# Kernel tuning notes

Measured on AMD Instinct MI355X. Metric: run time of the kernel, lower is better.

Reference implementation:

```python
import jax, jax.numpy as jnp
import numpy as np

N_NODES = 50000
N_EDGES = 1600000
D = 128
N_GRAPHS = 64


def gcn_conv(x, row, col, deg_inv_sqrt, W, b):
    # GCNConv: out_i = sum_{j->i} norm_ij * (x_j @ W) + norm_ii * (x_i @ W) + b
    # with self-loops folded in and norm_ij = d_i^{-1/2} d_j^{-1/2}
    h = x @ W  # [N, H]
    norm = deg_inv_sqrt[row] * deg_inv_sqrt[col]  # [E]
    msg = h[row] * norm[:, None]  # gather over source nodes
    agg = jax.ops.segment_sum(msg, col, num_segments=N_NODES)
    agg = agg + h * (deg_inv_sqrt * deg_inv_sqrt)[:, None]  # self-loop term
    return agg + b


def setup_inputs() -> dict:
    key = jax.random.key(0)
    ks = jax.random.split(key, 12)
    x = jax.random.normal(ks[0], (N_NODES, D), dtype=jnp.float32)
    edge_index = jax.random.randint(ks[1], (2, N_EDGES), 0, N_NODES, dtype=jnp.int32)
    batch = jnp.sort(jax.random.randint(ks[2], (N_NODES,), 0, N_GRAPHS, dtype=jnp.int32))
    s = 1.0 / np.sqrt(D)
    W1 = jax.random.uniform(ks[3], (D, D), jnp.float32, -s, s)
    b1 = jax.random.uniform(ks[4], (D,), jnp.float32, -s, s)
    W2 = jax.random.uniform(ks[5], (D, D), jnp.float32, -s, s)
    b2 = jax.random.uniform(ks[6], (D,), jnp.float32, -s, s)
    W3 = jax.random.uniform(ks[7], (D, D), jnp.float32, -s, s)
    b3 = jax.random.uniform(ks[8], (D,), jnp.float32, -s, s)
    Wf = jax.random.uniform(ks[9], (D, 1), jnp.float32, -s, s)
    bf = jax.random.uniform(ks[10], (1,), jnp.float32, -s, s)
    return {"x": x, "edge_index": edge_index, "batch": batch,
            "W1": W1, "b1": b1, "W2": W2, "b2": b2, "W3": W3, "b3": b3,
            "Wf": Wf, "bf": bf}


def reference(x, edge_index, batch, W1, b1, W2, b2, W3, b3, Wf, bf):
    row, col = edge_index[0], edge_index[1]  # source -> target
    ones = jnp.ones((N_EDGES,), dtype=jnp.float32)
    deg = jax.ops.segment_sum(ones, col, num_segments=N_NODES) + 1.0  # +1 self-loop
    deg_inv_sqrt = jax.lax.rsqrt(deg)

    h = x
    for W, b in ((W1, b1), (W2, b2), (W3, b3)):
        h = gcn_conv(h, row, col, deg_inv_sqrt, W, b)
        h = jax.nn.relu(h)  # dropout is identity in eval mode (p=0)

    # global mean pool over graphs
    sums = jax.ops.segment_sum(h, batch, num_segments=N_GRAPHS)
    counts = jax.ops.segment_sum(jnp.ones((N_NODES,), jnp.float32), batch, num_segments=N_GRAPHS)
    pooled = sums / jnp.maximum(counts, 1.0)[:, None]  # [G, D]

    out = pooled @ Wf + bf  # [G, 1]
    return jax.nn.sigmoid(out)
```

## Files before the change

kernel.cpp:

```cpp
#include <hip/hip_runtime.h>
#include <hip/hip_fp16.h>
#include <math.h>

#define N_NODES 50000
#define N_EDGES 1600000
#define DIM     128
#define N_GRAPHS 64

typedef unsigned int uint32;
typedef __attribute__((ext_vector_type(8))) short bf16x8;
typedef __attribute__((ext_vector_type(4))) float f32x4;

static __device__ __forceinline__ ushort f2b(float f) {
    uint32 u = __float_as_uint(f);
    uint32 r = (u + 0x7fffu + ((u >> 16) & 1u)) >> 16;
    return (ushort)r;
}
static __device__ __forceinline__ float b2f(ushort h) {
    return __uint_as_float(((uint32)h) << 16);
}
static __device__ __forceinline__ unsigned char f2e5(float f) {
    ushort hb = __half_as_ushort(__float2half(f));
    return (unsigned char)(((uint32)hb + 0x7fu + ((hb >> 8) & 1u)) >> 8);
}
union h2u_t { uint32 u; __half2 h; };
static __device__ __forceinline__ __half2 u2h2(uint32 u) { h2u_t t; t.u = u; return t.h; }
static __device__ __forceinline__ uint32 h2u(__half2 h)  { h2u_t t; t.h = h; return t.u; }
static __device__ __forceinline__ __half2 dec01(uint32 v) {
    return u2h2(__builtin_amdgcn_perm(v, 0u, 0x05000400u));
}
static __device__ __forceinline__ __half2 dec23(uint32 v) {
    return u2h2(__builtin_amdgcn_perm(v, 0u, 0x07000600u));
}
static __device__ __forceinline__ int permf(int p) { return ((p & 7) << 4) + (p >> 3); }

#define NBUK 196
#define CAP  16384
#define PB1  512
#define CHUNK1 (N_EDGES / PB1)

__global__ __launch_bounds__(256) void prep_k(const float* __restrict__ W1,
                                              const float* __restrict__ W2,
                                              const float* __restrict__ W3,
                                              ushort* __restrict__ wt,
                                              int* __restrict__ gfill,
                                              float* __restrict__ pooled) {
    int blk = blockIdx.x;
    if (blk < 192) {
        int w = blk >> 6;
        const float* W = (w == 0) ? W1 : (w == 1) ? W2 : W3;
        ushort* o = wt + w * (DIM * DIM);
        int t = (blk & 63) * 256 + threadIdx.x;
        int n = t >> 7, kp = t & 127;
        int f = (w == 0) ? kp : permf(kp);
        o[n * 128 + kp] = f2b(W[f * 128 + n]);
    } else if (blk == 192) {
        int t = threadIdx.x;
        if (t < NBUK) gfill[t] = t * CAP;
    } else {
        int t = (blk - 193) * 256 + threadIdx.x;
        if (t < N_GRAPHS * DIM + N_GRAPHS) pooled[t] = 0.f;
    }
}

__global__ __launch_bounds__(256) void bin_k(const int* __restrict__ col,
                                             const int* __restrict__ row,
                                             int* __restrict__ gfill,
                                             uint32* __restrict__ packed) {
    __shared__ int hist[NBUK];
    __shared__ int cur[NBUK];
    int tid = threadIdx.x;
    for (int t = tid; t < NBUK; t += 256) hist[t] = 0;
    __syncthreads();
    int start = blockIdx.x * CHUNK1, end = start + CHUNK1;
    for (int e = start + tid; e < end; e += 256)
        atomicAdd(&hist[col[e] >> 8], 1);
    __syncthreads();
    for (int t = tid; t < NBUK; t += 256) {
        int h = hist[t];
        cur[t] = h ? atomicAdd(&gfill[t], h) : 0;
    }
    __syncthreads();
    for (int e = start + tid; e < end; e += 256) {
        int c = col[e];
        int r = row[e];
        int pos = atomicAdd(&cur[c >> 8], 1);
        packed[pos] = ((uint32)(c & 255) << 16) | (uint32)r;
    }
}

__global__ __launch_bounds__(256) void bucket_k(const uint32* __restrict__ packed,
                                                const int* __restrict__ gfill,
                                                int* __restrict__ cnt,
                                                int* __restrict__ offs,
                                                float* __restrict__ dis,
                                                ushort* __restrict__ csr) {
    __shared__ int bsm[256];
    __shared__ int hist[256];
    __shared__ int sm[256];
    __shared__ int lo[256];
    __shared__ int rank[256];
    int b = blockIdx.x, tid = threadIdx.x;

    int bsz = (tid < NBUK) ? (gfill[tid] - tid * CAP) : 0;
    bsm[tid] = bsz;
    __syncthreads();
    for (int off = 1; off < 256; off <<= 1) {
        int u = 0;
        if (tid >= off) u = bsm[tid - off];
        __syncthreads();
        if (tid >= off) bsm[tid] += u;
        __syncthreads();
    }
    int size = gfill[b] - b * CAP;
    int gb = bsm[b] - size;

    const uint32* pk = packed + (size_t)b * CAP;
    hist[tid] = 0; rank[tid] = 0;
    __syncthreads();
    for (int e = tid; e < size; e += 256) atomicAdd(&hist[pk[e] >> 16], 1);
    __syncthreads();
    int h = hist[tid];
    sm[tid] = h;
    __syncthreads();
    for (int off = 1; off < 256; off <<= 1) {
        int u = 0;
        if (tid >= off) u = sm[tid - off];
        __syncthreads();
        if (tid >= off) sm[tid] += u;
        __syncthreads();
    }
    lo[tid] = sm[tid] - h;
    int node = (b << 8) + tid;
    if (node < N_NODES) {
        cnt[node]  = h;
        offs[node] = gb + lo[tid];
        dis[node]  = rsqrtf((float)h + 1.0f);
    }
    __syncthreads();
    for (int e = tid; e < size; e += 256) {
        uint32 p = pk[e];
        int cl = p >> 16;
        int r = atomicAdd(&rank[cl], 1);
        csr[gb + lo[cl] + r] = (ushort)(p & 0xffffu);
    }
}

__global__ __launch_bounds__(256) void conv_k(const float* __restrict__ x, ushort* __restrict__ xb) {
    int i = blockIdx.x * blockDim.x + threadIdx.x;
    const int n4 = N_NODES * DIM / 4;
    if (i >= n4) return;
    float4 v = ((const float4*)x)[i];
    ushort4 o;
    o.x = f2b(v.x); o.y = f2b(v.y); o.z = f2b(v.z); o.w = f2b(v.w);
    ((ushort4*)xb)[i] = o;
}

__global__ __launch_bounds__(256) void gemm_mfma_k(const ushort* __restrict__ xb,
                                                   const ushort* __restrict__ wt,
                                                   const float* __restrict__ dis,
                                                   unsigned char* __restrict__ gb) {
    int wid  = threadIdx.x >> 6;
    int lane = threadIdx.x & 63;
    int r0 = blockIdx.x * 128 + wid * 32;
    int m  = lane & 15;
    int kg = lane >> 4;

    int arow0 = r0 + m;
    int arow1 = r0 + 16 + m;
    if (arow0 >= N_NODES) arow0 = N_NODES - 1;
    if (arow1 >= N_NODES) arow1 = N_NODES - 1;
    const ushort* abase0 = xb + (size_t)arow0 * DIM + kg * 8;
    const ushort* abase1 = xb + (size_t)arow1 * DIM + kg * 8;
    const ushort* wbase  = wt + (size_t)m * DIM + kg * 8;

    f32x4 acc[2][8];
    #pragma unroll
    for (int hh = 0; hh < 2; ++hh)
        #pragma unroll
        for (int nt = 0; nt < 8; ++nt) acc[hh][nt] = (f32x4){0.f, 0.f, 0.f, 0.f};

    #pragma unroll
    for (int kb = 0; kb < 4; ++kb) {
        bf16x8 a0 = *(const bf16x8*)(abase0 + kb * 32);
        bf16x8 a1 = *(const bf16x8*)(abase1 + kb * 32);
        #pragma unroll
        for (int nt = 0; nt < 8; ++nt) {
            bf16x8 b = *(const bf16x8*)(wbase + (size_t)nt * 16 * DIM + kb * 32);
            acc[0][nt] = __builtin_amdgcn_mfma_f32_16x16x32_bf16(a0, b, acc[0][nt], 0, 0, 0);
            acc[1][nt] = __builtin_amdgcn_mfma_f32_16x16x32_bf16(a1, b, acc[1][nt], 0, 0, 0);
        }
    }

    #pragma unroll
    for (int hh = 0; hh < 2; ++hh) {
        int orow0 = r0 + hh * 16 + kg * 4;
        #pragma unroll
        for (int i = 0; i < 4; ++i) {
            int rr = orow0 + i;
            if (rr >= N_NODES) continue;
            float dsc = dis[rr];
            uint32 u0 = (uint32)f2e5(acc[hh][0][i] * dsc)
                      | ((uint32)f2e5(acc[hh][1][i] * dsc) << 8)
                      | ((uint32)f2e5(acc[hh][2][i] * dsc) << 16)
                      | ((uint32)f2e5(acc[hh][3][i] * dsc) << 24);
            uint32 u1 = (uint32)f2e5(acc[hh][4][i] * dsc)
                      | ((uint32)f2e5(acc[hh][5][i] * dsc) << 8)
                      | ((uint32)f2e5(acc[hh][6][i] * dsc) << 16)
                      | ((uint32)f2e5(acc[hh][7][i] * dsc) << 24);
            uint2 u = make_uint2(u0, u1);
            *(uint2*)(gb + (size_t)rr * DIM + m * 8) = u;
        }
    }
}

__global__ __launch_bounds__(256) void agg_k(const unsigned char* __restrict__ gb,
                                             const float* __restrict__ dis,
                                             const ushort* __restrict__ csr,
                                             const int* __restrict__ offs,
                                             const int* __restrict__ cnt,
                                             const float* __restrict__ bias,
                                             ushort* __restrict__ outb) {
    int lane = threadIdx.x & 63;
    int node = blockIdx.x * 4 + (threadIdx.x >> 6);
    if (node >= N_NODES) return;
    int hi = lane >> 5;
    uint32 c4 = (uint32)(lane & 31) << 2;
    const unsigned char* gq = gb + c4;

    uint32 sv = *(const uint32*)(gq + ((uint32)node << 7));
    if (hi) sv = 0;
    __half2 a0 = dec01(sv), b0 = dec23(sv);
    __half2 a1 = u2h2(0),   b1 = u2h2(0);

    int base = offs[node];
    int c = cnt[node];
    for (int s0 = 0; s0 < c; s0 += 64) {
        int rem = c - s0;
        int m = rem < 64 ? rem : 64;
        int idx = 0;
        if (lane < m) idx = csr[base + s0 + lane];
        int t = 0;
        for (; t + 16 <= m; t += 16) {
            uint32 v[8];
            #pragma unroll
            for (int p = 0; p < 8; ++p) {
                int j0 = __shfl(idx, t + 2 * p, 64);
                int j1 = __shfl(idx, t + 2 * p + 1, 64);
                int jr = hi ? j1 : j0;
                v[p] = *(const uint32*)(gq + ((uint32)jr << 7));
            }
            #pragma unroll
            for (int p = 0; p < 8; ++p) {
                if (p & 1) { a1 = __hadd2(a1, dec01(v[p])); b1 = __hadd2(b1, dec23(v[p])); }
                else       { a0 = __hadd2(a0, dec01(v[p])); b0 = __hadd2(b0, dec23(v[p])); }
            }
        }
        for (; t + 2 <= m; t += 2) {
            int j0 = __shfl(idx, t, 64);
            int j1 = __shfl(idx, t + 1, 64);
            int jr = hi ? j1 : j0;
            uint32 v = *(const uint32*)(gq + ((uint32)jr << 7));
            a0 = __hadd2(a0, dec01(v)); b0 = __hadd2(b0, dec23(v));
        }
        if (t < m) {
            int j = __shfl(idx, t, 64);
            uint32 v = *(const uint32*)(gq + ((uint32)j << 7));
            if (hi) v = 0;
            a0 = __hadd2(a0, dec01(v)); b0 = __hadd2(b0, dec23(v));
        }
    }

    __half2 accA = __hadd2(a0, a1);
    __half2 accB = __hadd2(b0, b1);
    accA = __hadd2(accA, u2h2((uint32)__shfl_xor((int)h2u(accA), 32, 64)));
    accB = __hadd2(accB, u2h2((uint32)__shfl_xor((int)h2u(accB), 32, 64)));

    if (hi == 0) {
        float f0 = __low2float(accA), f1 = __high2float(accA);
        float f2 = __low2float(accB), f3 = __high2float(accB);
        float d = dis[node];
        float bv0 = bias[permf(c4 + 0)];
        float bv1 = bias[permf(c4 + 1)];
        float bv2 = bias[permf(c4 + 2)];
        float bv3 = bias[permf(c4 + 3)];
        ushort4 o;
        o.x = f2b(fmaxf(fmaf(f0, d, bv0), 0.f));
        o.y = f2b(fmaxf(fmaf(f1, d, bv1), 0.f));
        o.z = f2b(fmaxf(fmaf(f2, d, bv2), 0.f));
        o.w = f2b(fmaxf(fmaf(f3, d, bv3), 0.f));
        *(ushort4*)(outb + ((size_t)node << 7) + c4) = o;
    }
}

#define POOL_BLOCKS 1024
__global__ __launch_bounds__(128) void pool_k(const ushort* __restrict__ hb,
                                              const int* __restrict__ batch,
                                              float* __restrict__ pooled,
                                              float* __restrict__ counts) {
    const int chunk = (N_NODES + POOL_BLOCKS - 1) / POOL_BLOCKS;
    int tid = threadIdx.x;
    int start = blockIdx.x * chunk;
    int end = start + chunk; if (end > N_NODES) end = N_NODES;
    if (start >= end) return;

    float acc = 0.f;
    int cur = batch[start];
    int cl = 0;
    for (int n = start; n < end; ++n) {
        int b = batch[n];
        if (b != cur) {
            atomicAdd(&pooled[cur * DIM + tid], acc);
            if (tid == 0) atomicAdd(&counts[cur], (float)cl);
            acc = 0.f; cl = 0; cur = b;
        }
        acc += b2f(hb[((size_t)n << 7) + tid]);
        ++cl;
    }
    atomicAdd(&pooled[cur * DIM + tid], acc);
    if (tid == 0) atomicAdd(&counts[cur], (float)cl);
}

__global__ void final_k(const float* __restrict__ pooled, const float* __restrict__ counts,
                        const float* __restrict__ Wf, const float* __restrict__ bf,
                        float* __restrict__ out) {
    __shared__ float sred[2];
    int gidx = blockIdx.x;
    int tid = threadIdx.x;
    float c = fmaxf(counts[gidx], 1.0f);
    float v = pooled[gidx * DIM + tid] / c * Wf[permf(tid)];
    for (int off = 32; off > 0; off >>= 1) v += __shfl_down(v, off, 64);
    if ((tid & 63) == 0) sred[tid >> 6] = v;
    __syncthreads();
    if (tid == 0) {
        float t = sred[0] + sred[1] + bf[0];
        out[gidx] = 1.0f / (1.0f + expf(-t));
    }
}

extern "C" void kernel_launch(void* const* d_in, const int* in_sizes, int n_in,
                              void* d_out, int out_size, void* d_ws, size_t ws_size,
                              hipStream_t stream) {
    const float* x     = (const float*)d_in[0];
    const int*   ei    = (const int*)d_in[1];
    const int*   batch = (const int*)d_in[2];
    const float* W1 = (const float*)d_in[3];  const float* b1 = (const float*)d_in[4];
    const float* W2 = (const float*)d_in[5];  const float* b2 = (const float*)d_in[6];
    const float* W3 = (const float*)d_in[7];  const float* b3 = (const float*)d_in[8];
    const float* Wf = (const float*)d_in[9];  const float* bf = (const float*)d_in[10];
    const int* rowp = ei;
    const int* colp = ei + N_EDGES;

    char* ws = (char*)d_ws;
    size_t o = 0;
    auto alloc = [&](size_t bytes) -> void* {
        void* p = ws + o;
        o += (bytes + 255) & ~(size_t)255;
        return p;
    };
    int*    cnt    = (int*)   alloc((size_t)N_NODES * 4);
    int*    offs   = (int*)   alloc((size_t)N_NODES * 4);
    int*    gfill  = (int*)   alloc(256 * 4);
    float*  dis    = (float*) alloc((size_t)N_NODES * 4);
    ushort* csr    = (ushort*)alloc((size_t)N_EDGES * 2);
    uint32* packed = (uint32*)alloc((size_t)NBUK * CAP * 4);
    float*  pooled = (float*) alloc((size_t)(N_GRAPHS * DIM + N_GRAPHS) * 4);
    ushort* wt     = (ushort*)alloc((size_t)3 * DIM * DIM * 2);
    unsigned char* bufA = (unsigned char*)alloc((size_t)N_NODES * DIM);
    ushort* bufB   = (ushort*)alloc((size_t)N_NODES * DIM * 2);
    float*  counts = pooled + N_GRAPHS * DIM;

    prep_k<<<226, 256, 0, stream>>>(W1, W2, W3, wt, gfill, pooled);
    bin_k<<<PB1, 256, 0, stream>>>(colp, rowp, gfill, packed);
    bucket_k<<<NBUK, 256, 0, stream>>>(packed, gfill, cnt, offs, dis, csr);

    conv_k<<<(N_NODES * DIM / 4 + 255) / 256, 256, 0, stream>>>(x, bufB);

    const int GB = (N_NODES + 127) / 128;

    gemm_mfma_k<<<GB, 256, 0, stream>>>(bufB, wt, dis, bufA);
    agg_k<<<(N_NODES + 3) / 4, 256, 0, stream>>>(bufA, dis, csr, offs, cnt, b1, bufB);
    gemm_mfma_k<<<GB, 256, 0, stream>>>(bufB, wt + DIM * DIM, dis, bufA);
    agg_k<<<(N_NODES + 3) / 4, 256, 0, stream>>>(bufA, dis, csr, offs, cnt, b2, bufB);
    gemm_mfma_k<<<GB, 256, 0, stream>>>(bufB, wt + 2 * DIM * DIM, dis, bufA);
    agg_k<<<(N_NODES + 3) / 4, 256, 0, stream>>>(bufA, dis, csr, offs, cnt, b3, bufB);

    pool_k<<<POOL_BLOCKS, 128, 0, stream>>>(bufB, batch, pooled, counts);
    final_k<<<N_GRAPHS, 128, 0, stream>>>(pooled, counts, Wf, bf, (float*)d_out);
}
```

Measured before the change: 239.5 us.

## Fuse x conversion into prep, cache edges in LDS, pack fp8 via cvt_pkrtz

Moves the fp32-to-bf16 conversion of x into the prep kernel, removing one kernel launch. bin_k now stages each block's col/row pairs in shared memory so the edge arrays are read from global memory once instead of twice. The GEMM epilogue replaces per-element fp16-to-e5 rounding with a packed cvt_pkrtz conversion plus byte permutes, cutting ALU work in the epilogue. The packed conversion rounds toward zero to fp16 before the e5m2 rounding step, which may slightly change numerics versus round-to-nearest.

```diff
diff --git a/kernel.cpp b/kernel.cpp
--- a/kernel.cpp
+++ b/kernel.cpp
@@ -22,6 +22,12 @@
 static __device__ __forceinline__ unsigned char f2e5(float f) {
     ushort hb = __half_as_ushort(__float2half(f));
     return (unsigned char)(((uint32)hb + 0x7fu + ((hb >> 8) & 1u)) >> 8);
+}
+static __device__ __forceinline__ uint32 pk2(float a, float b) {
+    auto h = __builtin_amdgcn_cvt_pkrtz(a, b);
+    uint32 u;
+    __builtin_memcpy(&u, &h, 4);
+    return u + 0x007F007Fu + ((u >> 8) & 0x00010001u);
 }
 union h2u_t { uint32 u; __half2 h; };
 static __device__ __forceinline__ __half2 u2h2(uint32 u) { h2u_t t; t.u = u; return t.h; }
@@ -39,53 +45,69 @@
 #define PB1  512
 #define CHUNK1 (N_EDGES / PB1)
 
-__global__ __launch_bounds__(256) void prep_k(const float* __restrict__ W1,
+#define PREP_CONV 6250
+__global__ __launch_bounds__(256) void prep_k(const float* __restrict__ x,
+                                              ushort* __restrict__ xb,
+                                              const float* __restrict__ W1,
                                               const float* __restrict__ W2,
                                               const float* __restrict__ W3,
                                               ushort* __restrict__ wt,
                                               int* __restrict__ gfill,
                                               float* __restrict__ pooled) {
     int blk = blockIdx.x;
-    if (blk < 192) {
-        int w = blk >> 6;
+    if (blk < PREP_CONV) {
+        int i = blk * 256 + threadIdx.x;
+        float4 v = ((const float4*)x)[i];
+        ushort4 o;
+        o.x = f2b(v.x); o.y = f2b(v.y); o.z = f2b(v.z); o.w = f2b(v.w);
+        ((ushort4*)xb)[i] = o;
+    } else if (blk < PREP_CONV + 192) {
+        int b2 = blk - PREP_CONV;
+        int w = b2 >> 6;
         const float* W = (w == 0) ? W1 : (w == 1) ? W2 : W3;
         ushort* o = wt + w * (DIM * DIM);
-        int t = (blk & 63) * 256 + threadIdx.x;
+        int t = (b2 & 63) * 256 + threadIdx.x;
         int n = t >> 7, kp = t & 127;
         int f = (w == 0) ? kp : permf(kp);
         o[n * 128 + kp] = f2b(W[f * 128 + n]);
-    } else if (blk == 192) {
+    } else if (blk == PREP_CONV + 192) {
         int t = threadIdx.x;
         if (t < NBUK) gfill[t] = t * CAP;
     } else {
-        int t = (blk - 193) * 256 + threadIdx.x;
+        int t = (blk - (PREP_CONV + 193)) * 256 + threadIdx.x;
         if (t < N_GRAPHS * DIM + N_GRAPHS) pooled[t] = 0.f;
     }
 }
+#define PREP_BLOCKS (PREP_CONV + 193 + 33)
 
 __global__ __launch_bounds__(256) void bin_k(const int* __restrict__ col,
                                              const int* __restrict__ row,
                                              int* __restrict__ gfill,
                                              uint32* __restrict__ packed) {
+    __shared__ uint32 epk[CHUNK1];
     __shared__ int hist[NBUK];
     __shared__ int cur[NBUK];
     int tid = threadIdx.x;
     for (int t = tid; t < NBUK; t += 256) hist[t] = 0;
     __syncthreads();
-    int start = blockIdx.x * CHUNK1, end = start + CHUNK1;
-    for (int e = start + tid; e < end; e += 256)
-        atomicAdd(&hist[col[e] >> 8], 1);
+    int start = blockIdx.x * CHUNK1;
+    for (int k = tid; k < CHUNK1; k += 256) {
+        int c = col[start + k];
+        int r = row[start + k];
+        epk[k] = ((uint32)c << 16) | (uint32)r;
+        atomicAdd(&hist[c >> 8], 1);
+    }
     __syncthreads();
     for (int t = tid; t < NBUK; t += 256) {
         int h = hist[t];
         cur[t] = h ? atomicAdd(&gfill[t], h) : 0;
     }
     __syncthreads();
-    for (int e = start + tid; e < end; e += 256) {
-        int c = col[e];
-        int r = row[e];
-        int pos = atomicAdd(&cur[c >> 8], 1);
-        packed[pos] = ((uint32)(c & 255) << 16) | (uint32)r;
+    for (int k = tid; k < CHUNK1; k += 256) {
+        uint32 p = epk[k];
+        int bu = p >> 24;
+        int pos = atomicAdd(&cur[bu], 1);
+        packed[pos] = p & 0x00FFFFFFu;
     }
 }
 
@@ -146,16 +168,6 @@
     }
 }
 
-__global__ __launch_bounds__(256) void conv_k(const float* __restrict__ x, ushort* __restrict__ xb) {
-    int i = blockIdx.x * blockDim.x + threadIdx.x;
-    const int n4 = N_NODES * DIM / 4;
-    if (i >= n4) return;
-    float4 v = ((const float4*)x)[i];
-    ushort4 o;
-    o.x = f2b(v.x); o.y = f2b(v.y); o.z = f2b(v.z); o.w = f2b(v.w);
-    ((ushort4*)xb)[i] = o;
-}
-
 __global__ __launch_bounds__(256) void gemm_mfma_k(const ushort* __restrict__ xb,
                                                    const ushort* __restrict__ wt,
                                                    const float* __restrict__ dis,
@@ -200,15 +212,13 @@
             int rr = orow0 + i;
             if (rr >= N_NODES) continue;
             float dsc = dis[rr];
-            uint32 u0 = (uint32)f2e5(acc[hh][0][i] * dsc)
-                      | ((uint32)f2e5(acc[hh][1][i] * dsc) << 8)
-                      | ((uint32)f2e5(acc[hh][2][i] * dsc) << 16)
-                      | ((uint32)f2e5(acc[hh][3][i] * dsc) << 24);
-            uint32 u1 = (uint32)f2e5(acc[hh][4][i] * dsc)
-                      | ((uint32)f2e5(acc[hh][5][i] * dsc) << 8)
-                      | ((uint32)f2e5(acc[hh][6][i] * dsc) << 16)
-                      | ((uint32)f2e5(acc[hh][7][i] * dsc) << 24);
-            uint2 u = make_uint2(u0, u1);
+            uint32 uA = pk2(acc[hh][0][i] * dsc, acc[hh][1][i] * dsc);
+            uint32 uB = pk2(acc[hh][2][i] * dsc, acc[hh][3][i] * dsc);
+            uint32 uC = pk2(acc[hh][4][i] * dsc, acc[hh][5][i] * dsc);
+            uint32 uD = pk2(acc[hh][6][i] * dsc, acc[hh][7][i] * dsc);
+            uint2 u;
+            u.x = __builtin_amdgcn_perm(uB, uA, 0x07050301u);
+            u.y = __builtin_amdgcn_perm(uD, uC, 0x07050301u);
             *(uint2*)(gb + (size_t)rr * DIM + m * 8) = u;
         }
     }
@@ -370,11 +380,9 @@
     ushort* bufB   = (ushort*)alloc((size_t)N_NODES * DIM * 2);
     float*  counts = pooled + N_GRAPHS * DIM;
 
-    prep_k<<<226, 256, 0, stream>>>(W1, W2, W3, wt, gfill, pooled);
+    prep_k<<<PREP_BLOCKS, 256, 0, stream>>>(x, bufB, W1, W2, W3, wt, gfill, pooled);
     bin_k<<<PB1, 256, 0, stream>>>(colp, rowp, gfill, packed);
     bucket_k<<<NBUK, 256, 0, stream>>>(packed, gfill, cnt, offs, dis, csr);
-
-    conv_k<<<(N_NODES * DIM / 4 + 255) / 256, 256, 0, stream>>>(x, bufB);
 
     const int GB = (N_NODES + 127) / 128;
 
```

New measurement: 232.2 us. 3.0% less time.
